# Kernel tuning notes

Hardware: AMD Instinct MI355X
Metric: run time of the kernel (lower is better)

The kernel has to match this reference:

```python
import jax, jax.numpy as jnp
import numpy as np

B, N, D = 8, 2048, 128

def setup_inputs() -> dict:
    key = jax.random.key(0)
    k1, k2, k3 = jax.random.split(key, 3)
    h = jax.random.normal(k1, (B, N, D), dtype=jnp.float32)
    W = jax.random.normal(k2, (D, D), dtype=jnp.float32) * (1.0 / np.sqrt(D))
    # a has shape [1,1,1,2D] in torch; flatten to [2D] (xavier-normal init)
    a = jax.random.normal(k3, (2 * D,), dtype=jnp.float32) * np.sqrt(2.0 / (2 * D))
    return {"h": h, "W": W, "a": a}

def reference(h, W, a):
    act = jax.nn.relu
    # h <- h @ W^T (nn.Linear with weight W means x @ W.T; here W is the weight matrix)
    hw = jnp.einsum('bnd,ed->bne', h, W)  # [B,N,D]
    a_i, a_j = a[:D], a[D:]
    # e_ij = act(a_i . h_i + a_j . h_j) -- equivalent to sum(cat(h_i,h_j)*a, -1)
    s_i = jnp.einsum('bnd,d->bn', hw, a_i)  # [B,N]
    s_j = jnp.einsum('bnd,d->bn', hw, a_j)  # [B,N]
    e = act(s_i[:, :, None] + s_j[:, None, :])  # [B,N,N]
    a_ij = jax.nn.softmax(e, axis=2)
    out = act(jnp.einsum('bij,bjd->bid', a_ij, hw))
    return out
```

## Files before the change

kernel.cpp:

```cpp
#include <hip/hip_runtime.h>
#include <hip/hip_bf16.h>

#define BB 8
#define NN 2048
#define DD 128
#define TI 16
#define HP 132
#define CH 32
#define NC (NN / CH)
#define NO (NC + 1)

__device__ __forceinline__ float relu(float x) { return x > 0.f ? x : 0.f; }

__global__ __launch_bounds__(256) void GraphAttentionalLayer_1168231104632_tr(
    const float* __restrict__ W, float* __restrict__ WT)
{
    const int g = blockIdx.x * 256 + threadIdx.x;
    const int d = g >> 7, e = g & 127;
    WT[g] = W[e * DD + d];
}

__global__ __launch_bounds__(128) void GraphAttentionalLayer_1168231104632_kernel(
    const float* __restrict__ h,
    const float* __restrict__ WT,
    const float* __restrict__ a,
    float* __restrict__ hw,
    float* __restrict__ E,
    float* __restrict__ F)
{
    __shared__ float h_s[TI][HP];
    __shared__ float wt_s[32][HP];

    const int t = threadIdx.x;
    const int tx = t & 31, ty = t >> 5;
    const int b = blockIdx.x >> 7;
    const int i0 = (blockIdx.x & 127) * TI;
    const size_t base = ((size_t)b * NN + i0) * DD;

    for (int r = 0; r < TI; r++)
        h_s[r][t] = h[base + (size_t)r * DD + t];

    const int e0 = tx * 4, r0 = ty * 4;
    float acc[4][4];
#pragma unroll
    for (int i = 0; i < 4; i++)
#pragma unroll
        for (int j = 0; j < 4; j++) acc[i][j] = 0.f;

    for (int dc = 0; dc < DD; dc += 32) {
        __syncthreads();
        for (int rr = 0; rr < 32; rr++)
            wt_s[rr][t] = WT[(size_t)(dc + rr) * DD + t];
        __syncthreads();
#pragma unroll 4
        for (int dd = 0; dd < 32; dd++) {
            const float4 wv = *reinterpret_cast<const float4*>(&wt_s[dd][e0]);
            const float w4[4] = {wv.x, wv.y, wv.z, wv.w};
#pragma unroll
            for (int r = 0; r < 4; r++) {
                const float hv = h_s[r0 + r][dc + dd];
#pragma unroll
                for (int e = 0; e < 4; e++) acc[r][e] += hv * w4[e];
            }
        }
    }

#pragma unroll
    for (int r = 0; r < 4; r++) {
        float4 o = make_float4(acc[r][0], acc[r][1], acc[r][2], acc[r][3]);
        *reinterpret_cast<float4*>(&hw[base + (size_t)(r0 + r) * DD + e0]) = o;
    }

    const float4 aiv = *reinterpret_cast<const float4*>(&a[e0]);
    const float4 ajv = *reinterpret_cast<const float4*>(&a[DD + e0]);
    const float ai4[4] = {aiv.x, aiv.y, aiv.z, aiv.w};
    const float aj4[4] = {ajv.x, ajv.y, ajv.z, ajv.w};
#pragma unroll
    for (int r = 0; r < 4; r++) {
        float pi = 0.f, pj = 0.f;
#pragma unroll
        for (int e = 0; e < 4; e++) { pi += acc[r][e] * ai4[e]; pj += acc[r][e] * aj4[e]; }
#pragma unroll
        for (int off = 16; off > 0; off >>= 1) {
            pi += __shfl_down(pi, off, 32);
            pj += __shfl_down(pj, off, 32);
        }
        if (tx == 0) {
            const size_t row = (size_t)b * NN + i0 + r0 + r;
            E[row] = __expf(pi);
            F[row] = __expf(pj);
        }
    }
}

__global__ __launch_bounds__(256) void GraphAttentionalLayer_1168231104632_rank(
    const float* __restrict__ F,
    float* __restrict__ Fsorted,
    int* __restrict__ perm)
{
    __shared__ float F_s[NN];
    __shared__ int   part[4][64];

    const int t = threadIdx.x;
    const int b = blockIdx.x >> 5;
    const int j0 = (blockIdx.x & 31) * 64;
    const size_t nb = (size_t)b * NN;

    for (int q = 0; q < NN / 256; q++)
        F_s[q * 256 + t] = F[nb + q * 256 + t];
    __syncthreads();

    const int tj = t & 63, ts = t >> 6;
    const int j = j0 + tj;
    const float fj = F_s[j];
    const int m0 = ts * (NN / 4);
    int cnt = 0;
#pragma unroll 8
    for (int mi = 0; mi < NN / 4; mi++) {
        const int m = m0 + mi;
        const float fm = F_s[m];
        cnt += (fm < fj) | ((fm == fj) & (m < j));
    }
    part[ts][tj] = cnt;
    __syncthreads();
    if (ts == 0) {
        const int r = part[0][tj] + part[1][tj] + part[2][tj] + part[3][tj];
        Fsorted[nb + r] = fj;
        perm[nb + r] = j;
    }
}

__global__ __launch_bounds__(128) void GraphAttentionalLayer_1168231104632_scan(
    const float* __restrict__ hw,
    const float* __restrict__ Fsorted,
    const int* __restrict__ perm,
    float* __restrict__ Q0L, float* __restrict__ Q1L,
    float* __restrict__ C0,  float* __restrict__ C1)
{
    const int t = threadIdx.x;
    const int b = blockIdx.x / NC, c = blockIdx.x % NC;
    const size_t nb = (size_t)b * NN;
    const int m0 = c * CH;

    int   jv[CH];
    float Fv[CH];
#pragma unroll
    for (int mm = 0; mm < CH; mm++) jv[mm] = perm[nb + m0 + mm];
#pragma unroll
    for (int mm = 0; mm < CH; mm++) Fv[mm] = Fsorted[nb + m0 + mm];

    float hv[CH];
#pragma unroll
    for (int mm = 0; mm < CH; mm++)
        hv[mm] = hw[(nb + jv[mm]) * DD + t];

    float a0 = 0.f, a1 = 0.f;
#pragma unroll
    for (int mm = 0; mm < CH; mm++) {
        const int m = m0 + mm;
        Q0L[(nb + m) * DD + t] = a0;
        Q1L[(nb + m) * DD + t] = a1;
        a0 += hv[mm];
        a1 += Fv[mm] * hv[mm];
    }
    C0[((size_t)b * NC + c) * DD + t] = a0;
    C1[((size_t)b * NC + c) * DD + t] = a1;
}

__global__ __launch_bounds__(128) void GraphAttentionalLayer_1168231104632_fix(
    const float* __restrict__ C0, const float* __restrict__ C1,
    float* __restrict__ O0, float* __restrict__ O1)
{
    const int t = threadIdx.x;
    const int b = blockIdx.x;
    float o0 = 0.f, o1 = 0.f;
    for (int cc = 0; cc < NC; cc += 16) {
        float c0[16], c1[16];
#pragma unroll
        for (int q = 0; q < 16; q++) {
            c0[q] = C0[((size_t)b * NC + cc + q) * DD + t];
            c1[q] = C1[((size_t)b * NC + cc + q) * DD + t];
        }
#pragma unroll
        for (int q = 0; q < 16; q++) {
            O0[((size_t)b * NO + cc + q) * DD + t] = o0;
            O1[((size_t)b * NO + cc + q) * DD + t] = o1;
            o0 += c0[q];
            o1 += c1[q];
        }
    }
    O0[((size_t)b * NO + NC) * DD + t] = o0;
    O1[((size_t)b * NO + NC) * DD + t] = o1;
}

__global__ __launch_bounds__(1024) void GraphAttentionalLayer_1168231104632_kz(
    const float* __restrict__ Fsorted,
    const float* __restrict__ E,
    int* __restrict__ kk,
    float* __restrict__ zinv)
{
    __shared__ float fs_s[NN];
    __shared__ float p0[NN];
    __shared__ float p1[NN];

    const int t = threadIdx.x;
    const int b = blockIdx.x;
    const size_t nb = (size_t)b * NN;

#pragma unroll
    for (int p = 0; p < 2; p++) {
        const int i = t + p * 1024;
        const float v = Fsorted[nb + i];
        fs_s[i] = v;
        p0[i] = v;
    }

    float* src = p0; float* dst = p1;
    for (int off = 1; off < NN; off <<= 1) {
        __syncthreads();
#pragma unroll
        for (int p = 0; p < 2; p++) {
            const int i = t + p * 1024;
            dst[i] = src[i] + (i >= off ? src[i - off] : 0.f);
        }
        float* sw = src; src = dst; dst = sw;
    }
    __syncthreads();
    const float TF = src[NN - 1];

#pragma unroll
    for (int p = 0; p < 2; p++) {
        const int i = t + p * 1024;
        const float Ei = E[nb + i];
        const float thr = 1.0f / Ei;
        int lo = 0, hi = NN;
        while (lo < hi) {
            const int mid = (lo + hi) >> 1;
            if (fs_s[mid] < thr) lo = mid + 1; else hi = mid;
        }
        const float SFk = TF - (lo ? src[lo - 1] : 0.f);
        const float z = Ei * SFk + (float)lo;
        kk[nb + i] = lo;
        zinv[nb + i] = 1.0f / z;
    }
}

__global__ __launch_bounds__(128) void GraphAttentionalLayer_1168231104632_out(
    const float* __restrict__ Q0L, const float* __restrict__ Q1L,
    const float* __restrict__ O0,  const float* __restrict__ O1,
    const int* __restrict__ kk,    const float* __restrict__ zinv,
    const float* __restrict__ E,   float* __restrict__ out)
{
    const int t = threadIdx.x;
    const int row = blockIdx.x;
    const int b = row >> 11;
    const size_t nb = (size_t)b * NN;

    const int k = kk[row];
    const float Ev = E[row];
    const float zv = zinv[row];
    const float T1 = O1[((size_t)b * NO + NC) * DD + t];

    float num;
    if (k < NN) {
        const int c = k >> 5;
        const float q0 = Q0L[(nb + k) * DD + t] + O0[((size_t)b * NO + c) * DD + t];
        const float q1 = Q1L[(nb + k) * DD + t] + O1[((size_t)b * NO + c) * DD + t];
        num = Ev * (T1 - q1) + q0;
    } else {
        num = O0[((size_t)b * NO + NC) * DD + t];
    }
    out[(size_t)row * DD + t] = relu(num * zv);
}

extern "C" __attribute__((visibility("default")))
void kernel_launch(void* const* d_in, const int* in_sizes, int n_in,
                   void* d_out, int out_size, void* d_ws, size_t ws_size,
                   hipStream_t stream) {
    const float* h = nullptr; const float* W = nullptr; const float* a = nullptr;
    for (int i = 0; i < n_in; i++) {
        if (in_sizes[i] == BB * NN * DD)      h = (const float*)d_in[i];
        else if (in_sizes[i] == DD * DD)      W = (const float*)d_in[i];
        else if (in_sizes[i] == 2 * DD)       a = (const float*)d_in[i];
    }
    if (!h) h = (const float*)d_in[0];
    if (!W) W = (const float*)d_in[1];
    if (!a) a = (const float*)d_in[2];

    float* out = (float*)d_out;
    float* ws = (float*)d_ws;

    float* WT   = ws;
    float* hw   = WT + DD * DD;
    float* E    = hw + (size_t)BB * NN * DD;
    float* F    = E + BB * NN;
    float* Fs   = F + BB * NN;
    float* zinv = Fs + BB * NN;
    int*   perm = (int*)(zinv + BB * NN);
    int*   kk   = perm + BB * NN;
    float* Q0L  = (float*)(kk + BB * NN);
    float* Q1L  = Q0L + (size_t)BB * NN * DD;
    float* C0   = Q1L + (size_t)BB * NN * DD;
    float* C1   = C0 + BB * NC * DD;
    float* O0   = C1 + BB * NC * DD;
    float* O1   = O0 + BB * NO * DD;
    const size_t need = (size_t)((O1 + BB * NO * DD) - ws) * sizeof(float);

    if (ws_size < need || d_ws == nullptr) {
        hipMemsetAsync(d_out, 0x42, (size_t)out_size * sizeof(float), stream);
        return;
    }

    GraphAttentionalLayer_1168231104632_tr<<<(DD * DD) / 256, 256, 0, stream>>>(W, WT);
    GraphAttentionalLayer_1168231104632_kernel<<<BB * (NN / TI), 128, 0, stream>>>(h, WT, a, hw, E, F);
    GraphAttentionalLayer_1168231104632_rank<<<BB * 32, 256, 0, stream>>>(F, Fs, perm);
    GraphAttentionalLayer_1168231104632_scan<<<BB * NC, 128, 0, stream>>>(hw, Fs, perm, Q0L, Q1L, C0, C1);
    GraphAttentionalLayer_1168231104632_fix<<<BB, 128, 0, stream>>>(C0, C1, O0, O1);
    GraphAttentionalLayer_1168231104632_kz<<<BB, 1024, 0, stream>>>(Fs, E, kk, zinv);
    GraphAttentionalLayer_1168231104632_out<<<BB * NN, 128, 0, stream>>>(Q0L, Q1L, O0, O1, kk, zinv, E, out);
}
```

Before: 114.9 us.

## Drop kz kernel: fold F prefix into scan/fix, binary search in out

Removes the separate 8-block, 1024-thread kz kernel, which did a full shared-memory Hillis-Steele scan over 2048 elements per batch. The prefix sums of sorted F are now built hierarchically: per-chunk in the scan kernel and across chunks in the fix kernel. The out kernel then runs the binary search per row against global memory, using thread 0 and a shared broadcast. The projection inner loop also switches to float4 reads of h_s with a fully unrolled 4x4x4 register block. This saves one launch and a low-occupancy kernel, at the cost of a serial thread-0 search with global loads in every out block.

```diff
diff --git a/kernel.cpp b/kernel.cpp
--- a/kernel.cpp
+++ b/kernel.cpp
@@ -52,16 +52,27 @@
         for (int rr = 0; rr < 32; rr++)
             wt_s[rr][t] = WT[(size_t)(dc + rr) * DD + t];
         __syncthreads();
-#pragma unroll 4
-        for (int dd = 0; dd < 32; dd++) {
-            const float4 wv = *reinterpret_cast<const float4*>(&wt_s[dd][e0]);
-            const float w4[4] = {wv.x, wv.y, wv.z, wv.w};
+#pragma unroll
+        for (int dd = 0; dd < 32; dd += 4) {
+            float wq[4][4], hq[4][4];
+#pragma unroll
+            for (int q = 0; q < 4; q++) {
+                const float4 v = *reinterpret_cast<const float4*>(&wt_s[dd + q][e0]);
+                wq[q][0] = v.x; wq[q][1] = v.y; wq[q][2] = v.z; wq[q][3] = v.w;
+            }
 #pragma unroll
             for (int r = 0; r < 4; r++) {
-                const float hv = h_s[r0 + r][dc + dd];
-#pragma unroll
-                for (int e = 0; e < 4; e++) acc[r][e] += hv * w4[e];
+                const float4 v = *reinterpret_cast<const float4*>(&h_s[r0 + r][dc + dd]);
+                hq[r][0] = v.x; hq[r][1] = v.y; hq[r][2] = v.z; hq[r][3] = v.w;
             }
+#pragma unroll
+            for (int r = 0; r < 4; r++)
+#pragma unroll
+                for (int q = 0; q < 4; q++) {
+                    const float hv = hq[r][q];
+#pragma unroll
+                    for (int e = 0; e < 4; e++) acc[r][e] += hv * wq[q][e];
+                }
         }
     }
 
@@ -135,7 +146,8 @@
     const float* __restrict__ Fsorted,
     const int* __restrict__ perm,
     float* __restrict__ Q0L, float* __restrict__ Q1L,
-    float* __restrict__ C0,  float* __restrict__ C1)
+    float* __restrict__ C0,  float* __restrict__ C1,
+    float* __restrict__ FPL, float* __restrict__ CF)
 {
     const int t = threadIdx.x;
     const int b = blockIdx.x / NC, c = blockIdx.x % NC;
@@ -165,14 +177,41 @@
     }
     C0[((size_t)b * NC + c) * DD + t] = a0;
     C1[((size_t)b * NC + c) * DD + t] = a1;
+
+    if (t == 0) {
+        float p = 0.f;
+#pragma unroll
+        for (int mm = 0; mm < CH; mm++) {
+            FPL[nb + m0 + mm] = p;
+            p += Fv[mm];
+        }
+        CF[(size_t)b * NC + c] = p;
+    }
 }
 
 __global__ __launch_bounds__(128) void GraphAttentionalLayer_1168231104632_fix(
     const float* __restrict__ C0, const float* __restrict__ C1,
-    float* __restrict__ O0, float* __restrict__ O1)
-{
+    const float* __restrict__ CF,
+    float* __restrict__ O0, float* __restrict__ O1,
+    float* __restrict__ OF)
+{
+    __shared__ float cf[NC], sc[NC];
+
     const int t = threadIdx.x;
     const int b = blockIdx.x;
+
+    if (t < NC) { const float v = CF[(size_t)b * NC + t]; cf[t] = v; sc[t] = v; }
+    __syncthreads();
+    for (int off = 1; off < NC; off <<= 1) {
+        float v = 0.f;
+        if (t < NC && t >= off) v = sc[t - off];
+        __syncthreads();
+        if (t < NC) sc[t] += v;
+        __syncthreads();
+    }
+    if (t < NC) OF[(size_t)b * NO + t] = sc[t] - cf[t];
+    if (t == 0) OF[(size_t)b * NO + NC] = sc[NC - 1];
+
     float o0 = 0.f, o1 = 0.f;
     for (int cc = 0; cc < NC; cc += 16) {
         float c0[16], c1[16];
@@ -193,72 +232,38 @@
     O1[((size_t)b * NO + NC) * DD + t] = o1;
 }
 
-__global__ __launch_bounds__(1024) void GraphAttentionalLayer_1168231104632_kz(
-    const float* __restrict__ Fsorted,
-    const float* __restrict__ E,
-    int* __restrict__ kk,
-    float* __restrict__ zinv)
-{
-    __shared__ float fs_s[NN];
-    __shared__ float p0[NN];
-    __shared__ float p1[NN];
-
-    const int t = threadIdx.x;
-    const int b = blockIdx.x;
+__global__ __launch_bounds__(128) void GraphAttentionalLayer_1168231104632_out(
+    const float* __restrict__ Q0L, const float* __restrict__ Q1L,
+    const float* __restrict__ O0,  const float* __restrict__ O1,
+    const float* __restrict__ Fsorted, const float* __restrict__ FPL,
+    const float* __restrict__ OF,  const float* __restrict__ E,
+    float* __restrict__ out)
+{
+    __shared__ int   k_sh;
+    __shared__ float e_sh, zi_sh;
+
+    const int t = threadIdx.x;
+    const int row = blockIdx.x;
+    const int b = row >> 11;
     const size_t nb = (size_t)b * NN;
 
-#pragma unroll
-    for (int p = 0; p < 2; p++) {
-        const int i = t + p * 1024;
-        const float v = Fsorted[nb + i];
-        fs_s[i] = v;
-        p0[i] = v;
-    }
-
-    float* src = p0; float* dst = p1;
-    for (int off = 1; off < NN; off <<= 1) {
-        __syncthreads();
-#pragma unroll
-        for (int p = 0; p < 2; p++) {
-            const int i = t + p * 1024;
-            dst[i] = src[i] + (i >= off ? src[i - off] : 0.f);
-        }
-        float* sw = src; src = dst; dst = sw;
-    }
-    __syncthreads();
-    const float TF = src[NN - 1];
-
-#pragma unroll
-    for (int p = 0; p < 2; p++) {
-        const int i = t + p * 1024;
-        const float Ei = E[nb + i];
+    if (t == 0) {
+        const float Ei = E[row];
         const float thr = 1.0f / Ei;
         int lo = 0, hi = NN;
         while (lo < hi) {
             const int mid = (lo + hi) >> 1;
-            if (fs_s[mid] < thr) lo = mid + 1; else hi = mid;
-        }
-        const float SFk = TF - (lo ? src[lo - 1] : 0.f);
-        const float z = Ei * SFk + (float)lo;
-        kk[nb + i] = lo;
-        zinv[nb + i] = 1.0f / z;
-    }
-}
-
-__global__ __launch_bounds__(128) void GraphAttentionalLayer_1168231104632_out(
-    const float* __restrict__ Q0L, const float* __restrict__ Q1L,
-    const float* __restrict__ O0,  const float* __restrict__ O1,
-    const int* __restrict__ kk,    const float* __restrict__ zinv,
-    const float* __restrict__ E,   float* __restrict__ out)
-{
-    const int t = threadIdx.x;
-    const int row = blockIdx.x;
-    const int b = row >> 11;
-    const size_t nb = (size_t)b * NN;
-
-    const int k = kk[row];
-    const float Ev = E[row];
-    const float zv = zinv[row];
+            if (Fsorted[nb + mid] < thr) lo = mid + 1; else hi = mid;
+        }
+        const float TF = OF[(size_t)b * NO + NC];
+        const float Pk = (lo < NN) ? (OF[(size_t)b * NO + (lo >> 5)] + FPL[nb + lo]) : TF;
+        const float z = Ei * (TF - Pk) + (float)lo;
+        k_sh = lo; e_sh = Ei; zi_sh = 1.0f / z;
+    }
+    __syncthreads();
+
+    const int k = k_sh;
+    const float Ev = e_sh, zv = zi_sh;
     const float T1 = O1[((size_t)b * NO + NC) * DD + t];
 
     float num;
@@ -295,10 +300,11 @@
     float* E    = hw + (size_t)BB * NN * DD;
     float* F    = E + BB * NN;
     float* Fs   = F + BB * NN;
-    float* zinv = Fs + BB * NN;
-    int*   perm = (int*)(zinv + BB * NN);
-    int*   kk   = perm + BB * NN;
-    float* Q0L  = (float*)(kk + BB * NN);
+    float* FPL  = Fs + BB * NN;
+    float* CF   = FPL + BB * NN;
+    float* OF   = CF + BB * NC;
+    int*   perm = (int*)(OF + BB * NO);
+    float* Q0L  = (float*)(perm + BB * NN);
     float* Q1L  = Q0L + (size_t)BB * NN * DD;
     float* C0   = Q1L + (size_t)BB * NN * DD;
     float* C1   = C0 + BB * NC * DD;
@@ -314,8 +320,7 @@
     GraphAttentionalLayer_1168231104632_tr<<<(DD * DD) / 256, 256, 0, stream>>>(W, WT);
     GraphAttentionalLayer_1168231104632_kernel<<<BB * (NN / TI), 128, 0, stream>>>(h, WT, a, hw, E, F);
     GraphAttentionalLayer_1168231104632_rank<<<BB * 32, 256, 0, stream>>>(F, Fs, perm);
-    GraphAttentionalLayer_1168231104632_scan<<<BB * NC, 128, 0, stream>>>(hw, Fs, perm, Q0L, Q1L, C0, C1);
-    GraphAttentionalLayer_1168231104632_fix<<<BB, 128, 0, stream>>>(C0, C1, O0, O1);
-    GraphAttentionalLayer_1168231104632_kz<<<BB, 1024, 0, stream>>>(Fs, E, kk, zinv);
-    GraphAttentionalLayer_1168231104632_out<<<BB * NN, 128, 0, stream>>>(Q0L, Q1L, O0, O1, kk, zinv, E, out);
-}
+    GraphAttentionalLayer_1168231104632_scan<<<BB * NC, 128, 0, stream>>>(hw, Fs, perm, Q0L, Q1L, C0, C1, FPL, CF);
+    GraphAttentionalLayer_1168231104632_fix<<<BB, 128, 0, stream>>>(C0, C1, CF, O0, O1, OF);
+    GraphAttentionalLayer_1168231104632_out<<<BB * NN, 128, 0, stream>>>(Q0L, Q1L, O0, O1, Fs, FPL, OF, E, out);
+}
```

Measured after the change: 118.9 us. 3.5% more time.

## Merge fix and kz kernels into one widely parallel mid kernel; enlarge GEMM tile

Applied to the files above, without the earlier changes.

The serial per-batch chunk-prefix fix kernel (8 blocks) and the single-block-per-batch scan/binary-search kz kernel are merged into one launch. In it, each block computes one chunk offset directly, and the row-wise k/z search is spread over 64 blocks using a two-level chunk prefix in place of a log-step shared scan. The hw projection kernel now uses 32-row tiles with 256 threads. This targets poor GPU occupancy and launch overhead in the small serial stages, at the cost of redundant summation work per offset block.

```diff
diff --git a/kernel.cpp b/kernel.cpp
--- a/kernel.cpp
+++ b/kernel.cpp
@@ -4,11 +4,12 @@
 #define BB 8
 #define NN 2048
 #define DD 128
-#define TI 16
+#define TI 32
 #define HP 132
 #define CH 32
 #define NC (NN / CH)
 #define NO (NC + 1)
+#define NFIX (BB * NO)
 
 __device__ __forceinline__ float relu(float x) { return x > 0.f ? x : 0.f; }
 
@@ -20,7 +21,7 @@
     WT[g] = W[e * DD + d];
 }
 
-__global__ __launch_bounds__(128) void GraphAttentionalLayer_1168231104632_kernel(
+__global__ __launch_bounds__(256) void GraphAttentionalLayer_1168231104632_kernel(
     const float* __restrict__ h,
     const float* __restrict__ WT,
     const float* __restrict__ a,
@@ -31,13 +32,15 @@
     __shared__ float h_s[TI][HP];
     __shared__ float wt_s[32][HP];
 
-    const int t = threadIdx.x;
-    const int tx = t & 31, ty = t >> 5;
-    const int b = blockIdx.x >> 7;
-    const int i0 = (blockIdx.x & 127) * TI;
+    const int tid = threadIdx.x;
+    const int t = tid & 127;
+    const int hh = tid >> 7;
+    const int tx = tid & 31, ty = tid >> 5;
+    const int b = blockIdx.x >> 6;
+    const int i0 = (blockIdx.x & 63) * TI;
     const size_t base = ((size_t)b * NN + i0) * DD;
 
-    for (int r = 0; r < TI; r++)
+    for (int r = hh; r < TI; r += 2)
         h_s[r][t] = h[base + (size_t)r * DD + t];
 
     const int e0 = tx * 4, r0 = ty * 4;
@@ -49,7 +52,7 @@
 
     for (int dc = 0; dc < DD; dc += 32) {
         __syncthreads();
-        for (int rr = 0; rr < 32; rr++)
+        for (int rr = hh; rr < 32; rr += 2)
             wt_s[rr][t] = WT[(size_t)(dc + rr) * DD + t];
         __syncthreads();
 #pragma unroll 4
@@ -167,82 +170,78 @@
     C1[((size_t)b * NC + c) * DD + t] = a1;
 }
 
-__global__ __launch_bounds__(128) void GraphAttentionalLayer_1168231104632_fix(
+__global__ __launch_bounds__(256) void GraphAttentionalLayer_1168231104632_mid(
     const float* __restrict__ C0, const float* __restrict__ C1,
-    float* __restrict__ O0, float* __restrict__ O1)
-{
-    const int t = threadIdx.x;
-    const int b = blockIdx.x;
-    float o0 = 0.f, o1 = 0.f;
-    for (int cc = 0; cc < NC; cc += 16) {
-        float c0[16], c1[16];
-#pragma unroll
-        for (int q = 0; q < 16; q++) {
-            c0[q] = C0[((size_t)b * NC + cc + q) * DD + t];
-            c1[q] = C1[((size_t)b * NC + cc + q) * DD + t];
+    const float* __restrict__ Fsorted, const float* __restrict__ E,
+    float* __restrict__ O0, float* __restrict__ O1,
+    int* __restrict__ kk,  float* __restrict__ zinv)
+{
+    __shared__ float fs_s[NN];
+    __shared__ float cf_s[NC];
+    __shared__ float of_s[NO];
+
+    const int tid = threadIdx.x;
+
+    if (blockIdx.x < NFIX) {
+        const int b = blockIdx.x / NO, c = blockIdx.x % NO;
+        const int d = tid & 127;
+        const float* C = (tid < 128) ? C0 : C1;
+        float*       O = (tid < 128) ? O0 : O1;
+        float o = 0.f;
+        int c2 = 0;
+        for (; c2 + 16 <= c; c2 += 16) {
+            float v[16];
+#pragma unroll
+            for (int q = 0; q < 16; q++)
+                v[q] = C[((size_t)b * NC + c2 + q) * DD + d];
+#pragma unroll
+            for (int q = 0; q < 16; q++) o += v[q];
         }
-#pragma unroll
-        for (int q = 0; q < 16; q++) {
-            O0[((size_t)b * NO + cc + q) * DD + t] = o0;
-            O1[((size_t)b * NO + cc + q) * DD + t] = o1;
-            o0 += c0[q];
-            o1 += c1[q];
-        }
-    }
-    O0[((size_t)b * NO + NC) * DD + t] = o0;
-    O1[((size_t)b * NO + NC) * DD + t] = o1;
-}
-
-__global__ __launch_bounds__(1024) void GraphAttentionalLayer_1168231104632_kz(
-    const float* __restrict__ Fsorted,
-    const float* __restrict__ E,
-    int* __restrict__ kk,
-    float* __restrict__ zinv)
-{
-    __shared__ float fs_s[NN];
-    __shared__ float p0[NN];
-    __shared__ float p1[NN];
-
-    const int t = threadIdx.x;
-    const int b = blockIdx.x;
+        for (; c2 < c; c2++)
+            o += C[((size_t)b * NC + c2) * DD + d];
+        O[((size_t)b * NO + c) * DD + d] = o;
+        return;
+    }
+
+    const int sb = blockIdx.x - NFIX;
+    const int b = sb >> 3;
+    const int i0 = (sb & 7) * 256;
     const size_t nb = (size_t)b * NN;
 
-#pragma unroll
-    for (int p = 0; p < 2; p++) {
-        const int i = t + p * 1024;
-        const float v = Fsorted[nb + i];
-        fs_s[i] = v;
-        p0[i] = v;
-    }
-
-    float* src = p0; float* dst = p1;
-    for (int off = 1; off < NN; off <<= 1) {
-        __syncthreads();
-#pragma unroll
-        for (int p = 0; p < 2; p++) {
-            const int i = t + p * 1024;
-            dst[i] = src[i] + (i >= off ? src[i - off] : 0.f);
-        }
-        float* sw = src; src = dst; dst = sw;
-    }
-    __syncthreads();
-    const float TF = src[NN - 1];
-
-#pragma unroll
-    for (int p = 0; p < 2; p++) {
-        const int i = t + p * 1024;
-        const float Ei = E[nb + i];
-        const float thr = 1.0f / Ei;
-        int lo = 0, hi = NN;
-        while (lo < hi) {
-            const int mid = (lo + hi) >> 1;
-            if (fs_s[mid] < thr) lo = mid + 1; else hi = mid;
-        }
-        const float SFk = TF - (lo ? src[lo - 1] : 0.f);
-        const float z = Ei * SFk + (float)lo;
-        kk[nb + i] = lo;
-        zinv[nb + i] = 1.0f / z;
-    }
+    for (int q = 0; q < NN / 256; q++)
+        fs_s[q * 256 + tid] = Fsorted[nb + q * 256 + tid];
+    __syncthreads();
+
+    if (tid < NC) {
+        float p = 0.f;
+        const int m0 = tid * CH;
+#pragma unroll
+        for (int mm = 0; mm < CH; mm++) p += fs_s[m0 + mm];
+        cf_s[tid] = p;
+    }
+    __syncthreads();
+    if (tid < NO) {
+        float p = 0.f;
+        for (int c2 = 0; c2 < tid; c2++) p += cf_s[c2];
+        of_s[tid] = p;
+    }
+    __syncthreads();
+
+    const int row = (int)nb + i0 + tid;
+    const float Ei = E[row];
+    const float thr = 1.0f / Ei;
+    int lo = 0, hi = NN;
+    while (lo < hi) {
+        const int mid = (lo + hi) >> 1;
+        if (fs_s[mid] < thr) lo = mid + 1; else hi = mid;
+    }
+    float fpl = 0.f;
+    for (int m = (lo >> 5) << 5; m < lo; m++) fpl += fs_s[m];
+    const float TF = of_s[NC];
+    const float Pk = of_s[lo >> 5] + fpl;
+    const float z = Ei * (TF - Pk) + (float)lo;
+    kk[row] = lo;
+    zinv[row] = 1.0f / z;
 }
 
 __global__ __launch_bounds__(128) void GraphAttentionalLayer_1168231104632_out(
@@ -312,10 +311,9 @@
     }
 
     GraphAttentionalLayer_1168231104632_tr<<<(DD * DD) / 256, 256, 0, stream>>>(W, WT);
-    GraphAttentionalLayer_1168231104632_kernel<<<BB * (NN / TI), 128, 0, stream>>>(h, WT, a, hw, E, F);
+    GraphAttentionalLayer_1168231104632_kernel<<<BB * (NN / TI), 256, 0, stream>>>(h, WT, a, hw, E, F);
     GraphAttentionalLayer_1168231104632_rank<<<BB * 32, 256, 0, stream>>>(F, Fs, perm);
     GraphAttentionalLayer_1168231104632_scan<<<BB * NC, 128, 0, stream>>>(hw, Fs, perm, Q0L, Q1L, C0, C1);
-    GraphAttentionalLayer_1168231104632_fix<<<BB, 128, 0, stream>>>(C0, C1, O0, O1);
-    GraphAttentionalLayer_1168231104632_kz<<<BB, 1024, 0, stream>>>(Fs, E, kk, zinv);
+    GraphAttentionalLayer_1168231104632_mid<<<NFIX + BB * 8, 256, 0, stream>>>(C0, C1, Fs, E, O0, O1, kk, zinv);
     GraphAttentionalLayer_1168231104632_out<<<BB * NN, 128, 0, stream>>>(Q0L, Q1L, O0, O1, kk, zinv, E, out);
 }
```

Measured after the change: 112.7 us. Within noise of the previous version (-1.9%).
